# Kernel tuning notes

Hardware: AMD Instinct MI355X
Metric: run time of the kernel (lower is better)

## Reference

```python
import jax, jax.numpy as jnp
import numpy as np

B, N, D, E, L = 8, 4096, 256, 65536, 1  # graphs, padded nodes, d_model, padded edges, num_layers


def setup_inputs() -> dict:
    key = jax.random.key(0)
    ks = jax.random.split(key, 9)
    x = jax.random.normal(ks[0], (B, N, D), dtype=jnp.float32)
    edge_index = jax.random.randint(ks[1], (B, 2, E), 0, N)
    edge_weight = jax.random.uniform(ks[2], (B, E), dtype=jnp.float32)
    mask = jax.random.randint(ks[3], (B, N), 0, 2).astype(jnp.int32)
    s = 1.0 / np.sqrt(D)
    # GatedGraphConv per-layer linear weight [L, D, D]
    W = jax.random.uniform(ks[4], (L, D, D), jnp.float32, -s, s)
    # GRUCell parameters (r, z, n stacked)
    W_ih = jax.random.uniform(ks[5], (3 * D, D), jnp.float32, -s, s)
    W_hh = jax.random.uniform(ks[6], (3 * D, D), jnp.float32, -s, s)
    b_ih = jax.random.uniform(ks[7], (3 * D,), jnp.float32, -s, s)
    b_hh = jax.random.uniform(ks[8], (3 * D,), jnp.float32, -s, s)
    return {"x": x, "edge_index": edge_index, "edge_weight": edge_weight,
            "mask": mask, "W": W, "W_ih": W_ih, "W_hh": W_hh,
            "b_ih": b_ih, "b_hh": b_hh}


def _gated_graph_conv(x, u, v, ew, W, W_ih, W_hh, b_ih, b_hh):
    """x:[B,N,D]; u,v:[B,E] src/dst indices; ew:[B,E] (already masked)."""
    h = x
    for l in range(L):
        m = jnp.einsum('bnd,de->bne', h, W[l])            # linear transform
        msg = jnp.take_along_axis(m, u[..., None], axis=1) * ew[..., None]  # [B,E,D]
        agg = jax.vmap(lambda ms, vi: jax.ops.segment_sum(ms, vi, num_segments=N))(msg, v)
        # GRUCell(input=agg, hidden=h)
        gi = agg @ W_ih.T + b_ih                          # [B,N,3D]
        gh = h @ W_hh.T + b_hh
        r = jax.nn.sigmoid(gi[..., :D] + gh[..., :D])
        z = jax.nn.sigmoid(gi[..., D:2 * D] + gh[..., D:2 * D])
        n = jnp.tanh(gi[..., 2 * D:] + r * gh[..., 2 * D:])
        h = (1.0 - z) * n + z * h
    return h


def reference(x, edge_index, edge_weight, mask, W, W_ih, W_hh, b_ih, b_hh):
    node_valid = mask > 0                                  # [B,N]
    u = edge_index[:, 0]                                   # source
    v = edge_index[:, 1]                                   # target
    # Drop edges touching invalid nodes: weight -> 0 (equivalent under sum aggr)
    e_valid = jnp.take_along_axis(node_valid, u, axis=1) & jnp.take_along_axis(node_valid, v, axis=1)
    ew = edge_weight * e_valid.astype(edge_weight.dtype)
    h = _gated_graph_conv(x, u, v, ew, W, W_ih, W_hh, b_ih, b_hh)
    # Invalid nodes stay zero (original writes only valid rows of a zeros output)
    return h * node_valid[..., None].astype(h.dtype)
```

## Files before the change

### kernel.cpp

```cpp
#include <hip/hip_runtime.h>
#include <math.h>

#define Bn 8
#define Nn 4096
#define Dn 256
#define En 65536

typedef __bf16 bf8 __attribute__((ext_vector_type(8)));
typedef float f4 __attribute__((ext_vector_type(4)));
typedef unsigned short us8 __attribute__((ext_vector_type(8)));

__device__ __forceinline__ float4 ld4(const float* p) { return *(const float4*)p; }

__device__ __forceinline__ unsigned short f2bf(float f) {
    union { float f; unsigned int u; } v; v.f = f;
    unsigned int r = v.u + 0x7fff + ((v.u >> 16) & 1);
    return (unsigned short)(r >> 16);
}
__device__ __forceinline__ float bf2f(unsigned short h) {
    union { unsigned int u; float f; } v; v.u = (unsigned int)h << 16;
    return v.f;
}


__device__ __forceinline__ void stage16c(const unsigned short* __restrict__ gchunk,
                                         int stride, char* ldschunk, int lane) {
    int u = lane >> 3, s = lane & 7;
    int xx = s ^ (u & 7);
    const unsigned short* g = gchunk + (size_t)(2 * u + (xx >> 2)) * stride + (xx & 3) * 8;
    __builtin_amdgcn_global_load_lds((const __attribute__((address_space(1))) void*)g,
                                     (__attribute__((address_space(3))) void*)ldschunk,
                                     16, 0, 0);
}

__device__ __forceinline__ bf8 fragld(const unsigned short* region, int r, int q) {
    int s = (((r & 1) << 2) | q) ^ ((r >> 1) & 7);
    return *(const bf8*)(region + (r >> 1) * 64 + s * 8);
}

__device__ __forceinline__ void ldswrite8(unsigned short* region, int r, int q,
                                          const unsigned short* vals) {
    int s = (((r & 1) << 2) | q) ^ ((r >> 1) & 7);
    *(us8*)(region + (r >> 1) * 64 + s * 8) = *(const us8*)vals;
}


__device__ void rowscan_piece(const int* __restrict__ mask, int* __restrict__ rowidx,
                              int* __restrict__ rowcnt, int* part) {
    int t = threadIdx.x;
    int base = t * 128;
    unsigned long long b0 = 0, b1 = 0;
    int s = 0;
#pragma unroll 8
    for (int i = 0; i < 64; i++) {
        int m = mask[base + i] > 0;
        b0 |= (unsigned long long)m << i; s += m;
    }
#pragma unroll 8
    for (int i = 0; i < 64; i++) {
        int m = mask[base + 64 + i] > 0;
        b1 |= (unsigned long long)m << i; s += m;
    }
    part[t] = s;
    __syncthreads();
    for (int st = 1; st < 256; st <<= 1) {
        int v = (t >= st) ? part[t - st] : 0;
        __syncthreads();
        part[t] += v;
        __syncthreads();
    }
    int run = part[t] - s;
    for (int i = 0; i < 64; i++)
        if ((b0 >> i) & 1) rowidx[run++] = base + i;
    for (int i = 0; i < 64; i++)
        if ((b1 >> i) & 1) rowidx[run++] = base + 64 + i;
    if (t == 255) rowcnt[0] = part[255];
}

__device__ void wf_piece(int wfi, const float* __restrict__ Wih, const float* __restrict__ W,
                         unsigned short* __restrict__ Ball, unsigned short* lds) {
    int t = threadIdx.x, lane = t & 63, w = t >> 6;
    int wr = w >> 1, wc = w & 1, q = lane >> 4, c16 = lane & 15;
    int o0 = (wfi % 6) * 128, d0b = (wfi / 6) * 64;
    f4 acc[4][2];
    f4 zz = {0.f, 0.f, 0.f, 0.f};
#pragma unroll
    for (int rt = 0; rt < 4; rt++)
#pragma unroll
        for (int ct = 0; ct < 2; ct++) acc[rt][ct] = zz;

    int r = t >> 1, half = t & 1;
    for (int k0 = 0; k0 < 256; k0 += 32) {
        const float* pa = Wih + (size_t)(o0 + r) * 256 + k0 + half * 16;
        float4 a0 = ld4(pa), a1 = ld4(pa + 4), a2 = ld4(pa + 8), a3 = ld4(pa + 12);
        float4 b0, b1, b2, b3;
        if (t < 128) {
            const float* pb = W + (size_t)(d0b + r) * 256 + k0 + half * 16;
            b0 = ld4(pb); b1 = ld4(pb + 4); b2 = ld4(pb + 8); b3 = ld4(pb + 12);
        }
        __syncthreads();
        unsigned short tmp[16];
        tmp[0] = f2bf(a0.x); tmp[1] = f2bf(a0.y); tmp[2] = f2bf(a0.z); tmp[3] = f2bf(a0.w);
        tmp[4] = f2bf(a1.x); tmp[5] = f2bf(a1.y); tmp[6] = f2bf(a1.z); tmp[7] = f2bf(a1.w);
        tmp[8] = f2bf(a2.x); tmp[9] = f2bf(a2.y); tmp[10] = f2bf(a2.z); tmp[11] = f2bf(a2.w);
        tmp[12] = f2bf(a3.x); tmp[13] = f2bf(a3.y); tmp[14] = f2bf(a3.z); tmp[15] = f2bf(a3.w);
        ldswrite8(lds, r, half * 2, tmp);
        ldswrite8(lds, r, half * 2 + 1, tmp + 8);
        if (t < 128) {
            unsigned short tb[16];
            tb[0] = f2bf(b0.x); tb[1] = f2bf(b0.y); tb[2] = f2bf(b0.z); tb[3] = f2bf(b0.w);
            tb[4] = f2bf(b1.x); tb[5] = f2bf(b1.y); tb[6] = f2bf(b1.z); tb[7] = f2bf(b1.w);
            tb[8] = f2bf(b2.x); tb[9] = f2bf(b2.y); tb[10] = f2bf(b2.z); tb[11] = f2bf(b2.w);
            tb[12] = f2bf(b3.x); tb[13] = f2bf(b3.y); tb[14] = f2bf(b3.z); tb[15] = f2bf(b3.w);
            ldswrite8(lds + 4096, r, half * 2, tb);
            ldswrite8(lds + 4096, r, half * 2 + 1, tb + 8);
        }
        __syncthreads();
        bf8 a[4];
#pragma unroll
        for (int rt = 0; rt < 4; rt++) a[rt] = fragld(lds, wr * 64 + rt * 16 + c16, q);
#pragma unroll
        for (int ct = 0; ct < 2; ct++) {
            bf8 b = fragld(lds + 4096, wc * 32 + ct * 16 + c16, q);
#pragma unroll
            for (int rt = 0; rt < 4; rt++)
                acc[rt][ct] = __builtin_amdgcn_mfma_f32_16x16x32_bf16(a[rt], b, acc[rt][ct], 0, 0, 0);
        }
    }
#pragma unroll
    for (int ct = 0; ct < 2; ct++) {
        int col = d0b + wc * 32 + ct * 16 + c16;
#pragma unroll
        for (int rt = 0; rt < 4; rt++) {
            int ob = o0 + wr * 64 + rt * 16 + q * 4;
#pragma unroll
            for (int i = 0; i < 4; i++)
                Ball[(size_t)(ob + i) * 512 + col] = f2bf(acc[rt][ct][i]);
        }
    }
}

__global__ __launch_bounds__(256) void setup_kernel(const int* __restrict__ ei,
                                                    const int* __restrict__ mask,
                                                    const float* __restrict__ Wih,
                                                    const float* __restrict__ W,
                                                    const float* __restrict__ Whh,
                                                    int* __restrict__ cnt,
                                                    int* __restrict__ rowidx,
                                                    int* __restrict__ rowcnt,
                                                    unsigned short* __restrict__ Ball,
                                                    float* __restrict__ out) {
    __shared__ __align__(16) unsigned short lds[6144];
    int b = blockIdx.x, t = threadIdx.x;
    if (b == 0) {
        rowscan_piece(mask, rowidx, rowcnt, (int*)lds);
        return;
    }
    if (b < 25) {
        wf_piece(b - 1, Wih, W, Ball, lds);
        return;
    }
    if (b < 217) {
        int i = ((b - 25) * 256 + t) * 4;
        float4 wv = ld4(Whh + i);
        int o = i >> 8, d = i & 255;
        ushort4 ov;
        ov.x = f2bf(wv.x); ov.y = f2bf(wv.y); ov.z = f2bf(wv.z); ov.w = f2bf(wv.w);
        *(ushort4*)(Ball + (size_t)o * 512 + 256 + d) = ov;
        return;
    }
    if (b < 2265) {
        int idx = (b - 217) * 256 + t;
        int bb = idx >> 16, e = idx & 65535;
        const int* eb = ei + (size_t)bb * 2 * En;
        int u = eb[e];
        int v = eb[En + e];
        const int* mb = mask + bb * Nn;
        if (mb[u] > 0 && mb[v] > 0) atomicAdd(&cnt[bb * Nn + v], 1);
        return;
    }
    {
        int zb = b - 2265;
        int r = zb * 8 + (t >> 5);
        if (mask[r] > 0) return;
        int col = (t & 31) * 8;
        float4 z = make_float4(0.f, 0.f, 0.f, 0.f);
        *(float4*)(out + (size_t)r * 256 + col) = z;
        *(float4*)(out + (size_t)r * 256 + col + 4) = z;
    }
}


__global__ __launch_bounds__(256) void scan_kernel(const int* __restrict__ cnt,
                                                   int* __restrict__ off,
                                                   int* __restrict__ cursor) {
    int b = blockIdx.x, t = threadIdx.x;
    __shared__ int chunk[256];
    int local[16];
    int s = 0;
    int base = b * Nn + t * 16;
#pragma unroll
    for (int i = 0; i < 16; i++) { local[i] = cnt[base + i]; s += local[i]; }
    chunk[t] = s;
    __syncthreads();
    for (int st = 1; st < 256; st <<= 1) {
        int v = (t >= st) ? chunk[t - st] : 0;
        __syncthreads();
        chunk[t] += v;
        __syncthreads();
    }
    int run = chunk[t] - s;
    int ob = b * (Nn + 1) + t * 16;
#pragma unroll
    for (int i = 0; i < 16; i++) {
        off[ob + i] = run;
        cursor[base + i] = run;
        run += local[i];
    }
    if (t == 255) off[b * (Nn + 1) + Nn] = run;
}

__global__ __launch_bounds__(256) void fill_kernel(const int* __restrict__ ei,
                                                   const int* __restrict__ mask,
                                                   const float* __restrict__ ew,
                                                   int* __restrict__ cursor,
                                                   int* __restrict__ csr_u,
                                                   float* __restrict__ csr_w) {
    int idx = blockIdx.x * 256 + threadIdx.x;
    int b = idx >> 16;
    int e = idx & 65535;
    const int* eb = ei + (size_t)b * 2 * En;
    int u = eb[e];
    int v = eb[En + e];
    const int* mb = mask + b * Nn;
    if (mb[u] > 0 && mb[v] > 0) {
        int pos = atomicAdd(&cursor[b * Nn + v], 1);
        csr_u[(size_t)b * En + pos] = u;
        csr_w[(size_t)b * En + pos] = ew[(size_t)b * En + e];
    }
}


__global__ __launch_bounds__(256) void agg_kernel(const float* __restrict__ x,
                                                  const int* __restrict__ off,
                                                  const int* __restrict__ csr_u,
                                                  const float* __restrict__ csr_w,
                                                  const int* __restrict__ rowidx,
                                                  const int* __restrict__ rowcnt,
                                                  unsigned short* __restrict__ Ac) {
    int wave = threadIdx.x >> 6, lane = threadIdx.x & 63;
    int i = blockIdx.x * 4 + wave;
    if (i >= rowcnt[0]) return;
    int v = rowidx[i];
    int b = v >> 12, n = v & 4095;
    int s = off[b * (Nn + 1) + n];
    int e = off[b * (Nn + 1) + n + 1];
    const int* cu = csr_u + (size_t)b * En;
    const float* cw = csr_w + (size_t)b * En;
    const float* Xb = x + (size_t)b * Nn * 256;
    float a0 = 0.f, a1 = 0.f, a2 = 0.f, a3 = 0.f;
    for (int j = s; j < e; j += 8) {
        int u[8]; float wv[8];
#pragma unroll
        for (int k = 0; k < 8; k++) {
            int jj = j + k;
            bool ok = jj < e;
            int idx = ok ? jj : s;
            u[k] = cu[idx];
            wv[k] = ok ? cw[idx] : 0.f;
        }
        float4 m[8];
#pragma unroll
        for (int k = 0; k < 8; k++) m[k] = ld4(Xb + (size_t)u[k] * 256 + lane * 4);
#pragma unroll
        for (int k = 0; k < 8; k++) {
            a0 += wv[k] * m[k].x; a1 += wv[k] * m[k].y;
            a2 += wv[k] * m[k].z; a3 += wv[k] * m[k].w;
        }
    }
    ushort4 o;
    o.x = f2bf(a0); o.y = f2bf(a1); o.z = f2bf(a2); o.w = f2bf(a3);
    *(ushort4*)(Ac + (size_t)i * 512 + lane * 4) = o;
    float4 xv = ld4(x + (size_t)v * 256 + lane * 4);
    ushort4 xo;
    xo.x = f2bf(xv.x); xo.y = f2bf(xv.y); xo.z = f2bf(xv.z); xo.w = f2bf(xv.w);
    *(ushort4*)(Ac + (size_t)i * 512 + 256 + lane * 4) = xo;
}


#define GRU_STAGE(kk, bufbase)                                                      \
    {                                                                               \
        _Pragma("unroll") for (int j = 0; j < 4; j++) {                             \
            int c = w * 4 + j;                                                      \
            const unsigned short* src;                                              \
            if (c < 4) {                                                            \
                src = Ac + (size_t)(row0 + c * 16) * 512 + (kk) * 32;               \
            } else {                                                                \
                int g = (c - 4) >> 2, cg = (c - 4) & 3;                             \
                src = Ball + (size_t)(g * 256 + d0 + cg * 16) * 512 + (kk) * 32;    \
            }                                                                       \
            stage16c(src, 512, (char*)(bufbase) + c * 1024, lane);                  \
        }                                                                           \
    }

#define GRU_COMPUTE(bufbase, ACCM)                                                  \
    {                                                                               \
        const unsigned short* rb = (bufbase);                                       \
        bf8 a0 = fragld(rb + (wr * 2) * 512, c16, q);                               \
        bf8 a1 = fragld(rb + (wr * 2 + 1) * 512, c16, q);                           \
        _Pragma("unroll") for (int ct = 0; ct < 2; ct++) {                          \
            int cg = wc * 2 + ct;                                                   \
            bf8 br = fragld(rb + (4 + cg) * 512, c16, q);                           \
            bf8 bz = fragld(rb + (8 + cg) * 512, c16, q);                           \
            bf8 bm = fragld(rb + (12 + cg) * 512, c16, q);                          \
            acc_r[0][ct] = __builtin_amdgcn_mfma_f32_16x16x32_bf16(a0, br, acc_r[0][ct], 0, 0, 0); \
            acc_r[1][ct] = __builtin_amdgcn_mfma_f32_16x16x32_bf16(a1, br, acc_r[1][ct], 0, 0, 0); \
            acc_z[0][ct] = __builtin_amdgcn_mfma_f32_16x16x32_bf16(a0, bz, acc_z[0][ct], 0, 0, 0); \
            acc_z[1][ct] = __builtin_amdgcn_mfma_f32_16x16x32_bf16(a1, bz, acc_z[1][ct], 0, 0, 0); \
            ACCM[0][ct] = __builtin_amdgcn_mfma_f32_16x16x32_bf16(a0, bm, ACCM[0][ct], 0, 0, 0);   \
            ACCM[1][ct] = __builtin_amdgcn_mfma_f32_16x16x32_bf16(a1, bm, ACCM[1][ct], 0, 0, 0);   \
        }                                                                           \
    }

__global__ __launch_bounds__(256, 4) void gru_kernel(const unsigned short* __restrict__ Ac,
                                                     const unsigned short* __restrict__ Ball,
                                                     const float* __restrict__ bih,
                                                     const float* __restrict__ bhh,
                                                     const int* __restrict__ rowidx,
                                                     const int* __restrict__ rowcnt,
                                                     float* __restrict__ out) {
    __shared__ __align__(16) unsigned short lds[16384];
    const int t = threadIdx.x;
    const int lane = t & 63, w = t >> 6;
    const int wr = w >> 1, wc = w & 1;
    const int q = lane >> 4, c16 = lane & 15;
    const int row0 = blockIdx.x * 64, d0 = blockIdx.y * 64;
    const int cnt = rowcnt[0];
    if (row0 >= cnt) return;

    f4 acc_r[2][2], acc_z[2][2], acc_gn[2][2], acc_hn[2][2];
    f4 zz = {0.f, 0.f, 0.f, 0.f};
#pragma unroll
    for (int rt = 0; rt < 2; rt++)
#pragma unroll
        for (int ct = 0; ct < 2; ct++) {
            acc_r[rt][ct] = zz; acc_z[rt][ct] = zz;
            acc_gn[rt][ct] = zz; acc_hn[rt][ct] = zz;
        }

    unsigned short* buf0 = lds;
    unsigned short* buf1 = lds + 8192;

    GRU_STAGE(0, buf0)
#pragma unroll
    for (int kk = 0; kk < 8; kk++) {
        __syncthreads();
        GRU_STAGE(kk + 1, (kk & 1) ? buf0 : buf1)
        GRU_COMPUTE((kk & 1) ? buf1 : buf0, acc_gn)
    }
#pragma unroll
    for (int kk = 8; kk < 16; kk++) {
        __syncthreads();
        if (kk < 15) GRU_STAGE(kk + 1, (kk & 1) ? buf0 : buf1)
        GRU_COMPUTE((kk & 1) ? buf1 : buf0, acc_hn)
    }

#pragma unroll
    for (int ct = 0; ct < 2; ct++) {
        int dd = d0 + wc * 32 + ct * 16 + c16;
        float b_r = bih[dd] + bhh[dd];
        float b_z = bih[dd + 256] + bhh[dd + 256];
        float b_gn = bih[dd + 512];
        float b_hn = bhh[dd + 512];
#pragma unroll
        for (int rt = 0; rt < 2; rt++) {
            int rbase = row0 + wr * 32 + rt * 16 + q * 4;
#pragma unroll
            for (int i = 0; i < 4; i++) {
                int rc = rbase + i;
                if (rc < cnt) {
                    float sr = acc_r[rt][ct][i] + b_r;
                    float sz = acc_z[rt][ct][i] + b_z;
                    float gn = acc_gn[rt][ct][i] + b_gn;
                    float hn = acc_hn[rt][ct][i] + b_hn;
                    float rg = 1.f / (1.f + __expf(-sr));
                    float zg = 1.f / (1.f + __expf(-sz));
                    float pre = gn + rg * hn;
                    float e2 = __expf(2.f * pre);
                    float ng = 1.f - 2.f / (e2 + 1.f);
                    float xv = bf2f(Ac[(size_t)rc * 512 + 256 + dd]);
                    float h = (1.f - zg) * ng + zg * xv;
                    int v = rowidx[rc];
                    out[(size_t)v * 256 + dd] = h;
                }
            }
        }
    }
}


extern "C" void kernel_launch(void* const* d_in, const int* in_sizes, int n_in,
                              void* d_out, int out_size, void* d_ws, size_t ws_size,
                              hipStream_t stream) {
    const float* x   = (const float*)d_in[0];
    const int*   ei  = (const int*)d_in[1];
    const float* ew  = (const float*)d_in[2];
    const int*   msk = (const int*)d_in[3];
    const float* W   = (const float*)d_in[4];
    const float* Wih = (const float*)d_in[5];
    const float* Whh = (const float*)d_in[6];
    const float* bih = (const float*)d_in[7];
    const float* bhh = (const float*)d_in[8];
    float* out = (float*)d_out;

    char* p = (char*)d_ws;
    unsigned short* Ac   = (unsigned short*)p; p += (size_t)Bn * Nn * 512 * 2;
    unsigned short* Ball = (unsigned short*)p; p += (size_t)768 * 512 * 2;
    int* cnt    = (int*)p;    p += (size_t)Bn * Nn * sizeof(int);
    int* off    = (int*)p;    p += (size_t)Bn * (Nn + 1) * sizeof(int);
    int* cursor = (int*)p;    p += (size_t)Bn * Nn * sizeof(int);
    int* csr_u  = (int*)p;    p += (size_t)Bn * En * sizeof(int);
    float* csr_w = (float*)p; p += (size_t)Bn * En * sizeof(float);
    int* rowidx = (int*)p;    p += (size_t)Bn * Nn * sizeof(int);
    int* rowcnt = (int*)p;    p += 128;

    hipMemsetAsync(cnt, 0, (size_t)Bn * Nn * sizeof(int), stream);
    setup_kernel<<<6361, 256, 0, stream>>>(ei, msk, Wih, W, Whh, cnt, rowidx, rowcnt,
                                           Ball, out);
    scan_kernel<<<Bn, 256, 0, stream>>>(cnt, off, cursor);
    fill_kernel<<<(Bn * En) / 256, 256, 0, stream>>>(ei, msk, ew, cursor, csr_u, csr_w);
    agg_kernel<<<(Bn * Nn) / 4, 256, 0, stream>>>(x, off, csr_u, csr_w, rowidx, rowcnt, Ac);
    gru_kernel<<<dim3(512, 4), 256, 0, stream>>>(Ac, Ball, bih, bhh, rowidx, rowcnt, out);
}
```

Baseline: 181.5 us.

## Gather from bf16 copy of x and enlarge GRU row tile to 128

Setup now also writes a bf16 copy of x, and the aggregation kernel gathers neighbour rows from it, halving the bytes of the random gather. The gather now reads values already rounded to bf16, which adds a small precision loss. The GRU GEMM kernel moves from 64 to 128 rows per block, so each wave holds 4 row tiles and reuses each staged weight fragment across more MFMAs. This cuts weight staging traffic but raises register and LDS use, and launch bounds drop from 4 to 2 blocks per CU.

Measured after the change: 189.2 us. 4.2% more time.

```diff
diff --git a/kernel.cpp b/kernel.cpp
--- a/kernel.cpp
+++ b/kernel.cpp
@@ -145,10 +145,12 @@
                                                     const float* __restrict__ Wih,
                                                     const float* __restrict__ W,
                                                     const float* __restrict__ Whh,
+                                                    const float* __restrict__ x,
                                                     int* __restrict__ cnt,
                                                     int* __restrict__ rowidx,
                                                     int* __restrict__ rowcnt,
                                                     unsigned short* __restrict__ Ball,
+                                                    unsigned short* __restrict__ xbf,
                                                     float* __restrict__ out) {
     __shared__ __align__(16) unsigned short lds[6144];
     int b = blockIdx.x, t = threadIdx.x;
@@ -179,7 +181,7 @@
         if (mb[u] > 0 && mb[v] > 0) atomicAdd(&cnt[bb * Nn + v], 1);
         return;
     }
-    {
+    if (b < 6361) {
         int zb = b - 2265;
         int r = zb * 8 + (t >> 5);
         if (mask[r] > 0) return;
@@ -187,6 +189,20 @@
         float4 z = make_float4(0.f, 0.f, 0.f, 0.f);
         *(float4*)(out + (size_t)r * 256 + col) = z;
         *(float4*)(out + (size_t)r * 256 + col + 4) = z;
+        return;
+    }
+    {
+        int idx = (b - 6361) * 256 + t;
+        size_t base = (size_t)idx * 16;
+        float4 v0 = ld4(x + base), v1 = ld4(x + base + 4);
+        float4 v2 = ld4(x + base + 8), v3 = ld4(x + base + 12);
+        us8 o0, o1;
+        o0[0] = f2bf(v0.x); o0[1] = f2bf(v0.y); o0[2] = f2bf(v0.z); o0[3] = f2bf(v0.w);
+        o0[4] = f2bf(v1.x); o0[5] = f2bf(v1.y); o0[6] = f2bf(v1.z); o0[7] = f2bf(v1.w);
+        o1[0] = f2bf(v2.x); o1[1] = f2bf(v2.y); o1[2] = f2bf(v2.z); o1[3] = f2bf(v2.w);
+        o1[4] = f2bf(v3.x); o1[5] = f2bf(v3.y); o1[6] = f2bf(v3.z); o1[7] = f2bf(v3.w);
+        *(us8*)(xbf + base) = o0;
+        *(us8*)(xbf + base + 8) = o1;
     }
 }
 
@@ -241,7 +257,7 @@
 }
 
 
-__global__ __launch_bounds__(256) void agg_kernel(const float* __restrict__ x,
+__global__ __launch_bounds__(256) void agg_kernel(const unsigned short* __restrict__ xbf,
                                                   const int* __restrict__ off,
                                                   const int* __restrict__ csr_u,
                                                   const float* __restrict__ csr_w,
@@ -257,7 +273,7 @@
     int e = off[b * (Nn + 1) + n + 1];
     const int* cu = csr_u + (size_t)b * En;
     const float* cw = csr_w + (size_t)b * En;
-    const float* Xb = x + (size_t)b * Nn * 256;
+    const unsigned short* Xb = xbf + ((size_t)(b << 12)) * 256;
     float a0 = 0.f, a1 = 0.f, a2 = 0.f, a3 = 0.f;
     for (int j = s; j < e; j += 8) {
         int u[8]; float wv[8];
@@ -269,34 +285,33 @@
             u[k] = cu[idx];
             wv[k] = ok ? cw[idx] : 0.f;
         }
-        float4 m[8];
-#pragma unroll
-        for (int k = 0; k < 8; k++) m[k] = ld4(Xb + (size_t)u[k] * 256 + lane * 4);
+        ushort4 m[8];
+#pragma unroll
+        for (int k = 0; k < 8; k++)
+            m[k] = *(const ushort4*)(Xb + (size_t)u[k] * 256 + lane * 4);
 #pragma unroll
         for (int k = 0; k < 8; k++) {
-            a0 += wv[k] * m[k].x; a1 += wv[k] * m[k].y;
-            a2 += wv[k] * m[k].z; a3 += wv[k] * m[k].w;
+            a0 += wv[k] * bf2f(m[k].x); a1 += wv[k] * bf2f(m[k].y);
+            a2 += wv[k] * bf2f(m[k].z); a3 += wv[k] * bf2f(m[k].w);
         }
     }
     ushort4 o;
     o.x = f2bf(a0); o.y = f2bf(a1); o.z = f2bf(a2); o.w = f2bf(a3);
     *(ushort4*)(Ac + (size_t)i * 512 + lane * 4) = o;
-    float4 xv = ld4(x + (size_t)v * 256 + lane * 4);
-    ushort4 xo;
-    xo.x = f2bf(xv.x); xo.y = f2bf(xv.y); xo.z = f2bf(xv.z); xo.w = f2bf(xv.w);
-    *(ushort4*)(Ac + (size_t)i * 512 + 256 + lane * 4) = xo;
+    *(ushort4*)(Ac + (size_t)i * 512 + 256 + lane * 4) =
+        *(const ushort4*)(xbf + (size_t)v * 256 + lane * 4);
 }
 
 
 #define GRU_STAGE(kk, bufbase)                                                      \
     {                                                                               \
-        _Pragma("unroll") for (int j = 0; j < 4; j++) {                             \
-            int c = w * 4 + j;                                                      \
+        _Pragma("unroll") for (int j = 0; j < 5; j++) {                             \
+            int c = w * 5 + j;                                                      \
             const unsigned short* src;                                              \
-            if (c < 4) {                                                            \
+            if (c < 8) {                                                            \
                 src = Ac + (size_t)(row0 + c * 16) * 512 + (kk) * 32;               \
             } else {                                                                \
-                int g = (c - 4) >> 2, cg = (c - 4) & 3;                             \
+                int g = (c - 8) >> 2, cg = (c - 8) & 3;                             \
                 src = Ball + (size_t)(g * 256 + d0 + cg * 16) * 512 + (kk) * 32;    \
             }                                                                       \
             stage16c(src, 512, (char*)(bufbase) + c * 1024, lane);                  \
@@ -306,42 +321,45 @@
 #define GRU_COMPUTE(bufbase, ACCM)                                                  \
     {                                                                               \
         const unsigned short* rb = (bufbase);                                       \
-        bf8 a0 = fragld(rb + (wr * 2) * 512, c16, q);                               \
-        bf8 a1 = fragld(rb + (wr * 2 + 1) * 512, c16, q);                           \
+        bf8 a[4];                                                                   \
+        _Pragma("unroll") for (int rt = 0; rt < 4; rt++)                            \
+            a[rt] = fragld(rb + (wr * 4 + rt) * 512, c16, q);                       \
         _Pragma("unroll") for (int ct = 0; ct < 2; ct++) {                          \
             int cg = wc * 2 + ct;                                                   \
-            bf8 br = fragld(rb + (4 + cg) * 512, c16, q);                           \
-            bf8 bz = fragld(rb + (8 + cg) * 512, c16, q);                           \
-            bf8 bm = fragld(rb + (12 + cg) * 512, c16, q);                          \
-            acc_r[0][ct] = __builtin_amdgcn_mfma_f32_16x16x32_bf16(a0, br, acc_r[0][ct], 0, 0, 0); \
-            acc_r[1][ct] = __builtin_amdgcn_mfma_f32_16x16x32_bf16(a1, br, acc_r[1][ct], 0, 0, 0); \
-            acc_z[0][ct] = __builtin_amdgcn_mfma_f32_16x16x32_bf16(a0, bz, acc_z[0][ct], 0, 0, 0); \
-            acc_z[1][ct] = __builtin_amdgcn_mfma_f32_16x16x32_bf16(a1, bz, acc_z[1][ct], 0, 0, 0); \
-            ACCM[0][ct] = __builtin_amdgcn_mfma_f32_16x16x32_bf16(a0, bm, ACCM[0][ct], 0, 0, 0);   \
-            ACCM[1][ct] = __builtin_amdgcn_mfma_f32_16x16x32_bf16(a1, bm, ACCM[1][ct], 0, 0, 0);   \
+            bf8 br = fragld(rb + (8 + cg) * 512, c16, q);                           \
+            bf8 bz = fragld(rb + (12 + cg) * 512, c16, q);                          \
+            bf8 bm = fragld(rb + (16 + cg) * 512, c16, q);                          \
+            _Pragma("unroll") for (int rt = 0; rt < 4; rt++) {                      \
+                acc_r[rt][ct] = __builtin_amdgcn_mfma_f32_16x16x32_bf16(            \
+                    a[rt], br, acc_r[rt][ct], 0, 0, 0);                             \
+                acc_z[rt][ct] = __builtin_amdgcn_mfma_f32_16x16x32_bf16(            \
+                    a[rt], bz, acc_z[rt][ct], 0, 0, 0);                             \
+                ACCM[rt][ct] = __builtin_amdgcn_mfma_f32_16x16x32_bf16(             \
+                    a[rt], bm, ACCM[rt][ct], 0, 0, 0);                              \
+            }                                                                       \
         }                                                                           \
     }
 
-__global__ __launch_bounds__(256, 4) void gru_kernel(const unsigned short* __restrict__ Ac,
+__global__ __launch_bounds__(256, 2) void gru_kernel(const unsigned short* __restrict__ Ac,
                                                      const unsigned short* __restrict__ Ball,
                                                      const float* __restrict__ bih,
                                                      const float* __restrict__ bhh,
                                                      const int* __restrict__ rowidx,
                                                      const int* __restrict__ rowcnt,
                                                      float* __restrict__ out) {
-    __shared__ __align__(16) unsigned short lds[16384];
+    __shared__ __align__(16) unsigned short lds[20480];
     const int t = threadIdx.x;
     const int lane = t & 63, w = t >> 6;
     const int wr = w >> 1, wc = w & 1;
     const int q = lane >> 4, c16 = lane & 15;
-    const int row0 = blockIdx.x * 64, d0 = blockIdx.y * 64;
+    const int row0 = blockIdx.x * 128, d0 = blockIdx.y * 64;
     const int cnt = rowcnt[0];
     if (row0 >= cnt) return;
 
-    f4 acc_r[2][2], acc_z[2][2], acc_gn[2][2], acc_hn[2][2];
+    f4 acc_r[4][2], acc_z[4][2], acc_gn[4][2], acc_hn[4][2];
     f4 zz = {0.f, 0.f, 0.f, 0.f};
 #pragma unroll
-    for (int rt = 0; rt < 2; rt++)
+    for (int rt = 0; rt < 4; rt++)
 #pragma unroll
         for (int ct = 0; ct < 2; ct++) {
             acc_r[rt][ct] = zz; acc_z[rt][ct] = zz;
@@ -349,7 +367,7 @@
         }
 
     unsigned short* buf0 = lds;
-    unsigned short* buf1 = lds + 8192;
+    unsigned short* buf1 = lds + 10240;
 
     GRU_STAGE(0, buf0)
 #pragma unroll
@@ -373,8 +391,8 @@
         float b_gn = bih[dd + 512];
         float b_hn = bhh[dd + 512];
 #pragma unroll
-        for (int rt = 0; rt < 2; rt++) {
-            int rbase = row0 + wr * 32 + rt * 16 + q * 4;
+        for (int rt = 0; rt < 4; rt++) {
+            int rbase = row0 + wr * 64 + rt * 16 + q * 4;
 #pragma unroll
             for (int i = 0; i < 4; i++) {
                 int rc = rbase + i;
@@ -415,6 +433,7 @@
 
     char* p = (char*)d_ws;
     unsigned short* Ac   = (unsigned short*)p; p += (size_t)Bn * Nn * 512 * 2;
+    unsigned short* xbf  = (unsigned short*)p; p += (size_t)Bn * Nn * Dn * 2;
     unsigned short* Ball = (unsigned short*)p; p += (size_t)768 * 512 * 2;
     int* cnt    = (int*)p;    p += (size_t)Bn * Nn * sizeof(int);
     int* off    = (int*)p;    p += (size_t)Bn * (Nn + 1) * sizeof(int);
@@ -425,10 +444,10 @@
     int* rowcnt = (int*)p;    p += 128;
 
     hipMemsetAsync(cnt, 0, (size_t)Bn * Nn * sizeof(int), stream);
-    setup_kernel<<<6361, 256, 0, stream>>>(ei, msk, Wih, W, Whh, cnt, rowidx, rowcnt,
-                                           Ball, out);
+    setup_kernel<<<8409, 256, 0, stream>>>(ei, msk, Wih, W, Whh, x, cnt, rowidx, rowcnt,
+                                           Ball, xbf, out);
     scan_kernel<<<Bn, 256, 0, stream>>>(cnt, off, cursor);
     fill_kernel<<<(Bn * En) / 256, 256, 0, stream>>>(ei, msk, ew, cursor, csr_u, csr_w);
-    agg_kernel<<<(Bn * Nn) / 4, 256, 0, stream>>>(x, off, csr_u, csr_w, rowidx, rowcnt, Ac);
-    gru_kernel<<<dim3(512, 4), 256, 0, stream>>>(Ac, Ball, bih, bhh, rowidx, rowcnt, out);
-}
+    agg_kernel<<<(Bn * Nn) / 4, 256, 0, stream>>>(xbf, off, csr_u, csr_w, rowidx, rowcnt, Ac);
+    gru_kernel<<<dim3(256, 4), 256, 0, stream>>>(Ac, Ball, bih, bhh, rowidx, rowcnt, out);
+}
```
